# Kernel tuning notes

Hardware: AMD Instinct MI355X
Metric: run time of the kernel (lower is better)

The kernel has to match this reference:

```python
import jax, jax.numpy as jnp
import numpy as np

N_ROLES = 6
EPS = 1e-5

def _ln(x, scale, bias):
    m = jnp.mean(x, axis=-1, keepdims=True)
    v = jnp.var(x, axis=-1, keepdims=True)
    return (x - m) * jax.lax.rsqrt(v + EPS) * scale + bias

def setup_inputs() -> dict:
    key = jax.random.key(0)
    ks = jax.random.split(key, 20)
    T, B, D_OBS, H, A = 32, 1024, 256, 512, 32
    inp = {
        'rnn_states': jax.random.normal(ks[0], (B, H), jnp.float32),
        'obs': jax.random.normal(ks[1], (T, B, D_OBS), jnp.float32),
        'resets': jnp.zeros((T, B), jnp.float32),
        'available_actions': jnp.ones((T, B, A), jnp.float32),
        'role_ids': jax.random.randint(ks[2], (T, B), 0, N_ROLES, jnp.int32),
        # feature norm over obs_dim
        'fn_scale': jnp.ones((D_OBS,), jnp.float32),
        'fn_bias': jnp.zeros((D_OBS,), jnp.float32),
        # base MLP: obs_dim->512->512, each followed by LayerNorm
        'W0': jax.random.normal(ks[3], (D_OBS, H), jnp.float32) * 0.02,
        'b0': jnp.zeros((H,), jnp.float32),
        'ln0_scale': jnp.ones((H,), jnp.float32),
        'ln0_bias': jnp.zeros((H,), jnp.float32),
        'W1': jax.random.normal(ks[4], (H, H), jnp.float32) * 0.02,
        'b1': jnp.zeros((H,), jnp.float32),
        'ln1_scale': jnp.ones((H,), jnp.float32),
        'ln1_bias': jnp.zeros((H,), jnp.float32),
        # per-role routes: obs_dim->128->H (stacked over roles)
        'Wr0': jax.random.normal(ks[5], (N_ROLES, D_OBS, 128), jnp.float32) * 0.02,
        'br0': jnp.zeros((N_ROLES, 128), jnp.float32),
        'Wr1': jax.random.normal(ks[6], (N_ROLES, 128, H), jnp.float32) * 0.02,
        'br1': jnp.zeros((N_ROLES, H), jnp.float32),
        # per-role heads: H->64->32->action_dim (stacked over roles)
        'Wh0': jax.random.normal(ks[7], (N_ROLES, H, 64), jnp.float32) * 0.02,
        'bh0': jnp.zeros((N_ROLES, 64), jnp.float32),
        'Wh1': jax.random.normal(ks[8], (N_ROLES, 64, 32), jnp.float32) * 0.02,
        'bh1': jnp.zeros((N_ROLES, 32), jnp.float32),
        'Wh2': jax.random.normal(ks[9], (N_ROLES, 32, A), jnp.float32) * 0.02,
        'bh2': jnp.zeros((N_ROLES, A), jnp.float32),
    }
    return inp

def _gather_by_role(all_values, role_ids):
    # all_values: (K, T, B, F); role_ids: (T, B) -> (T, B, F)
    idx = role_ids[None, :, :, None].astype(jnp.int32)
    return jnp.take_along_axis(all_values, idx, axis=0)[0]

def reference(rnn_states, obs, resets, available_actions, role_ids,
              fn_scale, fn_bias, W0, b0, ln0_scale, ln0_bias,
              W1, b1, ln1_scale, ln1_bias,
              Wr0, br0, Wr1, br1,
              Wh0, bh0, Wh1, bh1, Wh2, bh2):
    # feature normalization on raw obs
    obs_n = _ln(obs, fn_scale, fn_bias)
    # shared base MLP (relu + LayerNorm after each Dense)
    e = _ln(jax.nn.relu(obs_n @ W0 + b0), ln0_scale, ln0_bias)
    e = _ln(jax.nn.relu(e @ W1 + b1), ln1_scale, ln1_bias)
    # per-role pre-GRU residual routes on (normalized) obs
    r = jax.nn.relu(jnp.einsum('tbi,kih->ktbh', obs_n, Wr0) + br0[:, None, None, :])
    r = jax.nn.relu(jnp.einsum('ktbh,kho->ktbo', r, Wr1) + br1[:, None, None, :])
    e = e + _gather_by_role(r, role_ids)
    # no recurrent policy configured: rnn_states pass through
    # per-role heads -> all logits (K, T, B, A)
    h = jax.nn.relu(jnp.einsum('tbh,khf->ktbf', e, Wh0) + bh0[:, None, None, :])
    h = jax.nn.relu(jnp.einsum('ktbf,kfg->ktbg', h, Wh1) + bh1[:, None, None, :])
    all_logits = jnp.einsum('ktbg,kga->ktba', h, Wh2) + bh2[:, None, None, :]
    logits = _gather_by_role(all_logits, role_ids)
    logits = jnp.where(available_actions > 0.5, logits, jnp.full_like(logits, -1e10))
    return rnn_states, logits
```

## Files before the change

kernel.cpp:

```cpp
#include <hip/hip_runtime.h>
#include <stdint.h>

typedef unsigned short u16;
typedef unsigned int u32;

using bf16x8 = __attribute__((ext_vector_type(8))) short;
using f32x4  = __attribute__((ext_vector_type(4))) float;

#define DEVINL __device__ __forceinline__

DEVINL float b2f(u16 u) { return __builtin_bit_cast(float, (u32)u << 16); }
DEVINL u16 f2b(float f) {
  u32 u = __builtin_bit_cast(u32, f);
  u += 0x7FFFu + ((u >> 16) & 1u);
  return (u16)(u >> 16);
}

DEVINL void gll16(const u16* src, u16* dst) {
  __builtin_amdgcn_global_load_lds(
      (const __attribute__((address_space(1))) void*)(uintptr_t)src,
      (__attribute__((address_space(3))) void*)(uintptr_t)dst, 16, 0, 0);
}

#define MFMA __builtin_amdgcn_mfma_f32_16x16x32_bf16
#define NROLE 6

DEVINL void tp_tile(const float* __restrict__ s, u16* __restrict__ d,
                    int R, int C, int bx, int by, int z)
{
  __shared__ u16 tile[32][33];
  const size_t mstride = (size_t)R * C;
  s += (size_t)z * mstride;
  d += (size_t)z * mstride;
  int r0 = bx * 32, c0 = by * 32;
  int tx = threadIdx.x & 31, ty = threadIdx.x >> 5;
#pragma unroll
  for (int i = 0; i < 32; i += 8)
    tile[ty + i][tx] = f2b(s[(size_t)(r0 + ty + i) * C + (c0 + tx)]);
  __syncthreads();
#pragma unroll
  for (int i = 0; i < 32; i += 8)
    d[(size_t)(c0 + ty + i) * R + (r0 + tx)] = tile[tx][ty + i];
}

__global__ __launch_bounds__(256) void mega0(
    const float* W0, const float* W1, const float* Wr0, const float* Wr1, const float* Wh0,
    u16* W0t, u16* W1t, u16* Wr0t, u16* Wr1t, u16* Wh0t,
    const int* __restrict__ rid, int* __restrict__ blkCnt,
    const float* __restrict__ rnn, float* __restrict__ outRnn)
{
  int b = blockIdx.x;
  const int tid = threadIdx.x;
  if (b < 1152) {
    if (b < 128)      {            tp_tile(W0, W0t, 256, 512, b % 8,  b / 8, 0); }
    else if (b < 384) { b -= 128;  tp_tile(W1, W1t, 512, 512, b % 16, b / 16, 0); }
    else if (b < 576) { b -= 384;  int t = b / 8;  tp_tile(Wr0, Wr0t, 256, 128, b % 8,  t % 4,  t / 4); }
    else if (b < 960) { b -= 576;  int t = b / 4;  tp_tile(Wr1, Wr1t, 128, 512, b % 4,  t % 16, t / 16); }
    else              { b -= 960;  int t = b / 16; tp_tile(Wh0, Wh0t, 512, 64,  b % 16, t % 2,  t / 2); }
  } else if (b < 1280) {
    b -= 1152;
    __shared__ int h[NROLE];
    if (tid < NROLE) h[tid] = 0;
    __syncthreads();
    atomicAdd(&h[rid[b * 256 + tid]], 1);
    __syncthreads();
    if (tid < NROLE) blkCnt[b * NROLE + tid] = h[tid];
  } else {
    b -= 1280;
    const float4* src = (const float4*)rnn;
    float4* dst = (float4*)outRnn;
    int base = (b * 256 + tid) * 4;
#pragma unroll
    for (int i = 0; i < 4; ++i) dst[base + i] = src[base + i];
  }
}

__global__ __launch_bounds__(256, 2) void base2(
    const float* __restrict__ obs, const float* __restrict__ fn_s,
    const float* __restrict__ fn_b, const u16* __restrict__ W0t,
    const float* __restrict__ b0, const float* __restrict__ ln0sc,
    const float* __restrict__ ln0bi, const u16* __restrict__ W1t,
    const float* __restrict__ b1, const float* __restrict__ ln1sc,
    const float* __restrict__ ln1bi, u16* __restrict__ obs_n,
    u16* __restrict__ C,
    const int* __restrict__ rid, const int* __restrict__ blkCnt,
    int* __restrict__ bucket, int* __restrict__ baseArr, int* __restrict__ cntArr)
{
  __shared__ __align__(16) u16 smem[33792];
  const int tid = threadIdx.x;

  if (blockIdx.x >= 512) {
    const int bx = blockIdx.x - 512;
    int* c = (int*)smem;
    int* preArr = c + 768;
    int* scnt   = c + 776;
    int* sbase  = c + 784;
    int* h      = c + 792;
    for (int i = tid; i < 128 * NROLE; i += 256) c[i] = blkCnt[i];
    if (tid < NROLE) h[tid] = 0;
    __syncthreads();
    if (tid < NROLE) {
      int k = tid, run = 0, pre = 0;
      for (int b = 0; b < 128; ++b) { if (b == bx) pre = run; run += c[b * NROLE + k]; }
      scnt[k] = run; preArr[k] = pre;
    }
    __syncthreads();
    if (tid == 0) {
      int r = 0;
      for (int k = 0; k < NROLE; ++k) { sbase[k] = r; r += scnt[k]; }
    }
    __syncthreads();
    if (bx == 0 && tid < NROLE) { baseArr[tid] = sbase[tid]; cntArr[tid] = scnt[tid]; }
    int i = bx * 256 + tid;
    int k = rid[i];
    int pos = atomicAdd(&h[k], 1);
    bucket[sbase[k] + preArr[k] + pos] = i;
    return;
  }

  float* redS  = (float*)&smem[32768];
  float* redSS = redS + 256;
  const int rowBase = blockIdx.x * 64;
  const int lane = tid & 63, wave = tid >> 6;
  const int quad = lane >> 4, lm = lane & 15, l7 = lm & 7;
  const int wn = wave * 128;

  {
    const int r = tid >> 2, q = tid & 3;
    const float* xr = obs + (size_t)(rowBase + r) * 256 + q * 64;
    float x[64];
#pragma unroll
    for (int jj = 0; jj < 16; ++jj)
      *(float4*)&x[jj * 4] = *(const float4*)(xr + jj * 4);
    float s = 0.f, s2 = 0.f;
#pragma unroll
    for (int p = 0; p < 64; ++p) { s += x[p]; s2 += x[p] * x[p]; }
    s  += __shfl_xor(s, 1, 64);  s  += __shfl_xor(s, 2, 64);
    s2 += __shfl_xor(s2, 1, 64); s2 += __shfl_xor(s2, 2, 64);
    float m = s * (1.f / 256.f);
    float var = s2 * (1.f / 256.f) - m * m;
    float inv = rsqrtf(var + 1e-5f);
    const float* fs = fn_s + q * 64;
    const float* fb = fn_b + q * 64;
    u16* og = obs_n + (size_t)(rowBase + r) * 256 + q * 64;
#pragma unroll
    for (int j = 0; j < 8; ++j) {
      float4 fs0 = *(const float4*)(fs + j * 8);
      float4 fs1 = *(const float4*)(fs + j * 8 + 4);
      float4 fb0 = *(const float4*)(fb + j * 8);
      float4 fb1 = *(const float4*)(fb + j * 8 + 4);
      u16 yy[8] __attribute__((aligned(16)));
      yy[0] = f2b((x[j*8+0] - m) * inv * fs0.x + fb0.x);
      yy[1] = f2b((x[j*8+1] - m) * inv * fs0.y + fb0.y);
      yy[2] = f2b((x[j*8+2] - m) * inv * fs0.z + fb0.z);
      yy[3] = f2b((x[j*8+3] - m) * inv * fs0.w + fb0.w);
      yy[4] = f2b((x[j*8+4] - m) * inv * fs1.x + fb1.x);
      yy[5] = f2b((x[j*8+5] - m) * inv * fs1.y + fb1.y);
      yy[6] = f2b((x[j*8+6] - m) * inv * fs1.z + fb1.z);
      yy[7] = f2b((x[j*8+7] - m) * inv * fs1.w + fb1.w);
      int cch = q * 8 + j;
      *(uint4*)&smem[r * 256 + ((cch ^ (r & 7)) * 8)] = *(uint4*)yy;
      *(uint4*)(og + j * 8) = *(uint4*)yy;
    }
  }

  u32 bOff0[8];
#pragma unroll
  for (int j = 0; j < 8; ++j)
    bOff0[j] = (u32)(wn + j * 16 + lm) * 256u + (u32)(quad * 8);
  f32x4 acc[4][8] = {};
  bf16x8 bR[2][8];
#pragma unroll
  for (int p = 0; p < 2; ++p)
#pragma unroll
    for (int j = 0; j < 8; ++j)
      bR[p][j] = *(const bf16x8*)(W0t + bOff0[j] + p * 32);
  __syncthreads();

#pragma unroll
  for (int g = 0; g < 8; ++g) {
    bf16x8 cur[8];
#pragma unroll
    for (int j = 0; j < 8; ++j) cur[j] = bR[g & 1][j];
    if (g + 2 < 8) {
#pragma unroll
      for (int j = 0; j < 8; ++j)
        bR[g & 1][j] = *(const bf16x8*)(W0t + bOff0[j] + (g + 2) * 32);
    }
    const int kc = g * 4;
    bf16x8 af[4];
#pragma unroll
    for (int i2 = 0; i2 < 4; ++i2)
      af[i2] = *(const bf16x8*)&smem[(i2 * 16 + lm) * 256 + (((quad + kc) ^ l7) * 8)];
#pragma unroll
    for (int i2 = 0; i2 < 4; ++i2)
#pragma unroll
      for (int j = 0; j < 8; ++j)
        acc[i2][j] = MFMA(af[i2], cur[j], acc[i2][j], 0, 0, 0);
  }

  {
    float b0v[8];
#pragma unroll
    for (int j = 0; j < 8; ++j) b0v[j] = b0[wn + j * 16 + lm];
#pragma unroll
    for (int i2 = 0; i2 < 4; ++i2) {
#pragma unroll
      for (int r2 = 0; r2 < 4; ++r2) {
        float s = 0.f, ss = 0.f;
#pragma unroll
        for (int j = 0; j < 8; ++j) {
          float v = fmaxf(acc[i2][j][r2] + b0v[j], 0.f);
          acc[i2][j][r2] = v;
          s += v; ss += v * v;
        }
#pragma unroll
        for (int o = 1; o < 16; o <<= 1) { s += __shfl_xor(s, o, 64); ss += __shfl_xor(ss, o, 64); }
        if (lm == 0) {
          int row = i2 * 16 + quad * 4 + r2;
          redS[row * 4 + wave] = s;
          redSS[row * 4 + wave] = ss;
        }
      }
    }
  }
  __syncthreads();

  {
    float s0v[8], s0b[8];
#pragma unroll
    for (int j = 0; j < 8; ++j) {
      s0v[j] = ln0sc[wn + j * 16 + lm];
      s0b[j] = ln0bi[wn + j * 16 + lm];
    }
#pragma unroll
    for (int i2 = 0; i2 < 4; ++i2) {
#pragma unroll
      for (int r2 = 0; r2 < 4; ++r2) {
        int row = i2 * 16 + quad * 4 + r2;
        float ts  = redS[row * 4 + 0] + redS[row * 4 + 1] + redS[row * 4 + 2] + redS[row * 4 + 3];
        float tss = redSS[row * 4 + 0] + redSS[row * 4 + 1] + redSS[row * 4 + 2] + redSS[row * 4 + 3];
        float m = ts * (1.f / 512.f);
        float var = tss * (1.f / 512.f) - m * m;
        float inv = rsqrtf(var + 1e-5f);
#pragma unroll
        for (int j = 0; j < 8; ++j) {
          int col = wn + j * 16 + lm;
          float y = (acc[i2][j][r2] - m) * inv * s0v[j] + s0b[j];
          smem[row * 512 + (((col >> 3) ^ (row & 7)) * 8) + (col & 7)] = f2b(y);
        }
      }
    }
  }
  u32 bOff1[8];
#pragma unroll
  for (int j = 0; j < 8; ++j)
    bOff1[j] = (u32)(wn + j * 16 + lm) * 512u + (u32)(quad * 8);
#pragma unroll
  for (int p = 0; p < 2; ++p)
#pragma unroll
    for (int j = 0; j < 8; ++j)
      bR[p][j] = *(const bf16x8*)(W1t + bOff1[j] + p * 32);
  __syncthreads();

#pragma unroll
  for (int i2 = 0; i2 < 4; ++i2)
#pragma unroll
    for (int j = 0; j < 8; ++j)
      acc[i2][j] = (f32x4){0.f, 0.f, 0.f, 0.f};
#pragma unroll
  for (int g = 0; g < 16; ++g) {
    bf16x8 cur[8];
#pragma unroll
    for (int j = 0; j < 8; ++j) cur[j] = bR[g & 1][j];
    if (g + 2 < 16) {
#pragma unroll
      for (int j = 0; j < 8; ++j)
        bR[g & 1][j] = *(const bf16x8*)(W1t + bOff1[j] + (g + 2) * 32);
    }
    const int kc = g * 4;
    bf16x8 af[4];
#pragma unroll
    for (int i2 = 0; i2 < 4; ++i2)
      af[i2] = *(const bf16x8*)&smem[(i2 * 16 + lm) * 512 + (((quad + kc) ^ l7) * 8)];
#pragma unroll
    for (int i2 = 0; i2 < 4; ++i2)
#pragma unroll
      for (int j = 0; j < 8; ++j)
        acc[i2][j] = MFMA(af[i2], cur[j], acc[i2][j], 0, 0, 0);
  }

  {
    float b1v[8];
#pragma unroll
    for (int j = 0; j < 8; ++j) b1v[j] = b1[wn + j * 16 + lm];
#pragma unroll
    for (int i2 = 0; i2 < 4; ++i2) {
#pragma unroll
      for (int r2 = 0; r2 < 4; ++r2) {
        float s = 0.f, ss = 0.f;
#pragma unroll
        for (int j = 0; j < 8; ++j) {
          float v = fmaxf(acc[i2][j][r2] + b1v[j], 0.f);
          acc[i2][j][r2] = v;
          s += v; ss += v * v;
        }
#pragma unroll
        for (int o = 1; o < 16; o <<= 1) { s += __shfl_xor(s, o, 64); ss += __shfl_xor(ss, o, 64); }
        if (lm == 0) {
          int row = i2 * 16 + quad * 4 + r2;
          redS[row * 4 + wave] = s;
          redSS[row * 4 + wave] = ss;
        }
      }
    }
  }
  __syncthreads();

  {
    float s1v[8], s1b[8];
#pragma unroll
    for (int j = 0; j < 8; ++j) {
      s1v[j] = ln1sc[wn + j * 16 + lm];
      s1b[j] = ln1bi[wn + j * 16 + lm];
    }
#pragma unroll
    for (int i2 = 0; i2 < 4; ++i2) {
#pragma unroll
      for (int r2 = 0; r2 < 4; ++r2) {
        int row = i2 * 16 + quad * 4 + r2;
        float ts  = redS[row * 4 + 0] + redS[row * 4 + 1] + redS[row * 4 + 2] + redS[row * 4 + 3];
        float tss = redSS[row * 4 + 0] + redSS[row * 4 + 1] + redSS[row * 4 + 2] + redSS[row * 4 + 3];
        float m = ts * (1.f / 512.f);
        float var = tss * (1.f / 512.f) - m * m;
        float inv = rsqrtf(var + 1e-5f);
        size_t base = (size_t)(rowBase + row) * 512;
#pragma unroll
        for (int j = 0; j < 8; ++j) {
          int col = wn + j * 16 + lm;
          float y = (acc[i2][j][r2] - m) * inv * s1v[j] + s1b[j];
          C[base + col] = f2b(y);
        }
      }
    }
  }
}

__global__ __launch_bounds__(256, 4) void route_head(
    const u16* __restrict__ obs_n, const u16* __restrict__ e,
    const u16* __restrict__ Wr0t, const float* __restrict__ br0,
    const u16* __restrict__ Wr1t, const float* __restrict__ br1,
    const u16* __restrict__ Wh0t, const float* __restrict__ bh0,
    const float* __restrict__ Wh1, const float* __restrict__ bh1,
    const float* __restrict__ Wh2, const float* __restrict__ bh2,
    const float* __restrict__ avail,
    const int* __restrict__ bucket, const int* __restrict__ baseArr,
    const int* __restrict__ cntArr, float* __restrict__ outLogits)
{
  __shared__ __align__(16) u16 sm[20480];
  const int tid = threadIdx.x;

  int cA0, cA1, cA2, cA3, cA4, cA5, bA0, bA1, bA2, bA3, bA4, bA5;
  {
    int4 ca = *(const int4*)cntArr;  int2 cb = *(const int2*)(cntArr + 4);
    int4 ba = *(const int4*)baseArr; int2 bb = *(const int2*)(baseArr + 4);
    cA0 = ca.x; cA1 = ca.y; cA2 = ca.z; cA3 = ca.w; cA4 = cb.x; cA5 = cb.y;
    bA0 = ba.x; bA1 = ba.y; bA2 = ba.z; bA3 = ba.w; bA4 = bb.x; bA5 = bb.y;
  }
  int role = -1, rem = blockIdx.x, cnt = 0, roleBase = 0;
#define TRY_ROLE(k, ck, bk)                                        \
  if (role < 0) {                                                  \
    int tiles = ((ck) + 31) >> 5;                                  \
    if (rem < tiles) { role = (k); cnt = (ck); roleBase = (bk); }  \
    else rem -= tiles;                                             \
  }
  TRY_ROLE(0, cA0, bA0) TRY_ROLE(1, cA1, bA1) TRY_ROLE(2, cA2, bA2)
  TRY_ROLE(3, cA3, bA3) TRY_ROLE(4, cA4, bA4) TRY_ROLE(5, cA5, bA5)
#undef TRY_ROLE
  if (role < 0) return;
  const int limit = cnt;
  const int rowBase = rem * 32;

  const int lane = tid & 63, wave = tid >> 6;
  const int quad = lane >> 4, lm = lane & 15, l7 = lm & 7;

#pragma unroll
  for (int r = 0; r < 8; ++r) {
    int lrow = r * 4 + wave;
    int i = rowBase + lrow;
    if (i >= limit) i = rowBase;
    int grow = bucket[roleBase + i];
    int chunk = tid & 63;
    int sw = (chunk & 56) | ((chunk ^ lrow) & 7);
    gll16(e + (u32)grow * 512u + (u32)(sw * 8), &sm[r * 2048 + wave * 512]);
  }

  int growA0, growA1;
  {
    int i0 = rowBase + lm;        if (i0 >= limit) i0 = rowBase;
    int i1 = rowBase + 16 + lm;   if (i1 >= limit) i1 = rowBase;
    growA0 = bucket[roleBase + i0];
    growA1 = bucket[roleBase + i1];
  }
  const u16* Ag0 = obs_n + (size_t)growA0 * 256;
  const u16* Ag1 = obs_n + (size_t)growA1 * 256;

  const int wn0 = wave * 32;
  const u16* B0 = Wr0t + (size_t)role * 128 * 256;
  f32x4 acc0[2][2] = {};
  bf16x8 b0R[2][2];
#pragma unroll
  for (int p = 0; p < 2; ++p)
#pragma unroll
    for (int j = 0; j < 2; ++j)
      b0R[p][j] = *(const bf16x8*)(B0 + (u32)(wn0 + j * 16 + lm) * 256u + (u32)(quad * 8 + p * 32));
  bf16x8 aR[4][2];
#pragma unroll
  for (int p = 0; p < 4; ++p) {
    aR[p][0] = *(const bf16x8*)(Ag0 + (u32)(quad * 8 + p * 32));
    aR[p][1] = *(const bf16x8*)(Ag1 + (u32)(quad * 8 + p * 32));
  }
  float bias0[2] = { br0[role * 128 + wn0 + lm], br0[role * 128 + wn0 + 16 + lm] };
#pragma unroll
  for (int it = 0; it < 8; ++it) {
    bf16x8 a0 = aR[it & 3][0], a1 = aR[it & 3][1];
    bf16x8 cur0 = b0R[it & 1][0], cur1 = b0R[it & 1][1];
    if (it + 2 < 8) {
#pragma unroll
      for (int j = 0; j < 2; ++j)
        b0R[it & 1][j] = *(const bf16x8*)(B0 + (u32)(wn0 + j * 16 + lm) * 256u + (u32)(quad * 8 + (it + 2) * 32));
    }
    if (it + 4 < 8) {
      aR[it & 3][0] = *(const bf16x8*)(Ag0 + (u32)(quad * 8 + (it + 4) * 32));
      aR[it & 3][1] = *(const bf16x8*)(Ag1 + (u32)(quad * 8 + (it + 4) * 32));
    }
    acc0[0][0] = MFMA(a0, cur0, acc0[0][0], 0, 0, 0);
    acc0[0][1] = MFMA(a0, cur1, acc0[0][1], 0, 0, 0);
    acc0[1][0] = MFMA(a1, cur0, acc0[1][0], 0, 0, 0);
    acc0[1][1] = MFMA(a1, cur1, acc0[1][1], 0, 0, 0);
  }
  u16* r1 = sm + 16384;
#pragma unroll
  for (int i2 = 0; i2 < 2; ++i2) {
#pragma unroll
    for (int r2 = 0; r2 < 4; ++r2) {
      int row = i2 * 16 + quad * 4 + r2;
#pragma unroll
      for (int j = 0; j < 2; ++j) {
        int col = wn0 + j * 16 + lm;
        float v = fmaxf(acc0[i2][j][r2] + bias0[j], 0.f);
        r1[row * 128 + (((col >> 3) ^ (row & 7)) * 8) + (col & 7)] = f2b(v);
      }
    }
  }
  __syncthreads();

  const int wn1 = wave * 128;
  const u16* B1 = Wr1t + (size_t)role * 512 * 128;
#pragma unroll
  for (int h = 0; h < 2; ++h) {
    const int wnh = wn1 + h * 64;
    float b1v[4];
#pragma unroll
    for (int j = 0; j < 4; ++j) b1v[j] = br1[role * 512 + wnh + j * 16 + lm];
    f32x4 acc1[2][4] = {};
    bf16x8 b1P[4];
#pragma unroll
    for (int j = 0; j < 4; ++j)
      b1P[j] = *(const bf16x8*)(B1 + (u32)(wnh + j * 16 + lm) * 128u + (u32)(quad * 8));
#pragma unroll
    for (int kk = 0; kk < 128; kk += 32) {
      bf16x8 b1N[4];
      if (kk + 32 < 128) {
#pragma unroll
        for (int j = 0; j < 4; ++j)
          b1N[j] = *(const bf16x8*)(B1 + (u32)(wnh + j * 16 + lm) * 128u + (u32)(quad * 8 + kk + 32));
      }
      const int kc = kk >> 3;
      bf16x8 af[2];
#pragma unroll
      for (int i2 = 0; i2 < 2; ++i2)
        af[i2] = *(const bf16x8*)&r1[(i2 * 16 + lm) * 128 + (((quad + kc) ^ l7) * 8)];
#pragma unroll
      for (int i2 = 0; i2 < 2; ++i2)
#pragma unroll
        for (int j = 0; j < 4; ++j)
          acc1[i2][j] = MFMA(af[i2], b1P[j], acc1[i2][j], 0, 0, 0);
      if (kk + 32 < 128) {
#pragma unroll
        for (int j = 0; j < 4; ++j) b1P[j] = b1N[j];
      }
    }
#pragma unroll
    for (int i2 = 0; i2 < 2; ++i2) {
#pragma unroll
      for (int r2 = 0; r2 < 4; ++r2) {
        int row = i2 * 16 + quad * 4 + r2;
#pragma unroll
        for (int j = 0; j < 4; ++j) {
          int col = wnh + j * 16 + lm;
          int addr = row * 512 + (((col >> 3) ^ (row & 7)) * 8) + (col & 7);
          float v = fmaxf(acc1[i2][j][r2] + b1v[j], 0.f) + b2f(sm[addr]);
          sm[addr] = f2b(v);
        }
      }
    }
  }
  __syncthreads();

  const int wn2 = wave * 16;
  const u16* B2 = Wh0t + (size_t)role * 64 * 512;
  float b2v = bh0[role * 64 + wn2 + lm];
  f32x4 acc2[2] = {};
  bf16x8 b2R[4];
#pragma unroll
  for (int p = 0; p < 4; ++p)
    b2R[p] = *(const bf16x8*)(B2 + (u32)(wn2 + lm) * 512u + (u32)(quad * 8 + p * 32));
#pragma unroll
  for (int it = 0; it < 16; ++it) {
    bf16x8 cur = b2R[it & 3];
    if (it + 4 < 16)
      b2R[it & 3] = *(const bf16x8*)(B2 + (u32)(wn2 + lm) * 512u + (u32)(quad * 8 + (it + 4) * 32));
    const int kc = it * 4;
    bf16x8 af[2];
#pragma unroll
    for (int i2 = 0; i2 < 2; ++i2)
      af[i2] = *(const bf16x8*)&sm[(i2 * 16 + lm) * 512 + (((quad + kc) ^ l7) * 8)];
#pragma unroll
    for (int i2 = 0; i2 < 2; ++i2)
      acc2[i2] = MFMA(af[i2], cur, acc2[i2], 0, 0, 0);
  }
  u16* h0s = sm + 16384;
#pragma unroll
  for (int i2 = 0; i2 < 2; ++i2) {
#pragma unroll
    for (int r2 = 0; r2 < 4; ++r2) {
      int row = i2 * 16 + quad * 4 + r2;
      int col = wn2 + lm;
      h0s[row * 68 + col] = f2b(fmaxf(acc2[i2][r2] + b2v, 0.f));
    }
  }
  __syncthreads();

  {
    float* h1s = (float*)&sm[16384];
    const int r = tid >> 3;
    const int n0 = (tid & 7) * 4;
    const bool valid = (rowBase + r) < limit;
    const float* W1k = Wh1 + (size_t)role * 64 * 32;
    const float* W2k = Wh2 + (size_t)role * 32 * 32;
    float4 a1 = *(const float4*)(bh1 + role * 32 + n0);
#pragma unroll 8
    for (int j = 0; j < 64; ++j) {
      float hj = b2f(h0s[r * 68 + j]);
      float4 wv = *(const float4*)(W1k + j * 32 + n0);
      a1.x += hj * wv.x; a1.y += hj * wv.y; a1.z += hj * wv.z; a1.w += hj * wv.w;
    }
    a1.x = fmaxf(a1.x, 0.f); a1.y = fmaxf(a1.y, 0.f);
    a1.z = fmaxf(a1.z, 0.f); a1.w = fmaxf(a1.w, 0.f);
    __syncthreads();
    h1s[r * 36 + n0 + 0] = a1.x;
    h1s[r * 36 + n0 + 1] = a1.y;
    h1s[r * 36 + n0 + 2] = a1.z;
    h1s[r * 36 + n0 + 3] = a1.w;
    __syncthreads();
    float4 a2 = *(const float4*)(bh2 + role * 32 + n0);
#pragma unroll 8
    for (int n = 0; n < 32; ++n) {
      float hn = h1s[r * 36 + n];
      float4 wv = *(const float4*)(W2k + n * 32 + n0);
      a2.x += hn * wv.x; a2.y += hn * wv.y; a2.z += hn * wv.z; a2.w += hn * wv.w;
    }
    if (valid) {
      int g = bucket[roleBase + rowBase + r];
      float4 av = *(const float4*)(avail + (size_t)g * 32 + n0);
      float4 o;
      o.x = (av.x > 0.5f) ? a2.x : -1e10f;
      o.y = (av.y > 0.5f) ? a2.y : -1e10f;
      o.z = (av.z > 0.5f) ? a2.z : -1e10f;
      o.w = (av.w > 0.5f) ? a2.w : -1e10f;
      *(float4*)(outLogits + (size_t)g * 32 + n0) = o;
    }
  }
}

extern "C" void kernel_launch(void* const* d_in, const int* in_sizes, int n_in,
                              void* d_out, int out_size, void* d_ws, size_t ws_size,
                              hipStream_t stream)
{
  const float* rnn  = (const float*)d_in[0];
  const float* obs  = (const float*)d_in[1];
  const float* avail= (const float*)d_in[3];
  const int*   rid  = (const int*)d_in[4];
  const float* fn_s = (const float*)d_in[5];
  const float* fn_b = (const float*)d_in[6];
  const float* W0   = (const float*)d_in[7];
  const float* b0   = (const float*)d_in[8];
  const float* ln0s = (const float*)d_in[9];
  const float* ln0b = (const float*)d_in[10];
  const float* W1   = (const float*)d_in[11];
  const float* b1   = (const float*)d_in[12];
  const float* ln1s = (const float*)d_in[13];
  const float* ln1b = (const float*)d_in[14];
  const float* Wr0  = (const float*)d_in[15];
  const float* br0  = (const float*)d_in[16];
  const float* Wr1  = (const float*)d_in[17];
  const float* br1  = (const float*)d_in[18];
  const float* Wh0  = (const float*)d_in[19];
  const float* bh0  = (const float*)d_in[20];
  const float* Wh1  = (const float*)d_in[21];
  const float* bh1  = (const float*)d_in[22];
  const float* Wh2  = (const float*)d_in[23];
  const float* bh2  = (const float*)d_in[24];

  const int ROWS = 32768;

  char* w = (char*)d_ws;
  auto carve = [&](size_t bytes) { char* p = w; w += (bytes + 255) & ~(size_t)255; return p; };
  u16* obs_n  = (u16*)carve((size_t)ROWS * 256 * 2);
  u16* bufB   = (u16*)carve((size_t)ROWS * 512 * 2);
  u16* W0t    = (u16*)carve((size_t)512 * 256 * 2);
  u16* W1t    = (u16*)carve((size_t)512 * 512 * 2);
  u16* Wr0t   = (u16*)carve((size_t)6 * 128 * 256 * 2);
  u16* Wr1t   = (u16*)carve((size_t)6 * 512 * 128 * 2);
  u16* Wh0t   = (u16*)carve((size_t)6 * 64 * 512 * 2);
  int* bucket = (int*)carve((size_t)ROWS * 4);
  int* blkCnt = (int*)carve((size_t)128 * NROLE * 4);
  int* baseArr= (int*)carve(256);
  int* cntArr = (int*)carve(256);

  float* outLogits = (float*)d_out + (size_t)1024 * 512;

  mega0<<<1408, 256, 0, stream>>>(W0, W1, Wr0, Wr1, Wh0, W0t, W1t, Wr0t, Wr1t, Wh0t,
                                  rid, blkCnt, rnn, (float*)d_out);

  base2<<<640, 256, 0, stream>>>(obs, fn_s, fn_b, W0t, b0, ln0s, ln0b,
                                 W1t, b1, ln1s, ln1b, obs_n, bufB,
                                 rid, blkCnt, bucket, baseArr, cntArr);

  route_head<<<1029, 256, 0, stream>>>(obs_n, bufB, Wr0t, br0, Wr1t, br1, Wh0t, bh0,
                                       Wh1, bh1, Wh2, bh2, avail,
                                       bucket, baseArr, cntArr, outLogits);
}
```

Measured before the change: 263.9 us.

## Halve base MLP row tile to 32 rows for higher occupancy and staged output

The base MLP kernel now processes 32 rows per block instead of 64, using half the shared memory and accumulator registers, with launch bounds raised to 4 blocks per SM and a grid of 1152 blocks. The weight prefetch is reduced from a two-deep register buffer to single-step double buffering. The final LayerNorm output is staged in shared memory and written to global memory with coalesced 16-byte stores. The intent is more resident waves and more blocks to hide latency. The cost is that each block reloads the full W0/W1 weights for fewer rows, doubling weight traffic per output row.

```diff
diff --git a/kernel.cpp b/kernel.cpp
--- a/kernel.cpp
+++ b/kernel.cpp
@@ -75,7 +75,7 @@
   }
 }
 
-__global__ __launch_bounds__(256, 2) void base2(
+__global__ __launch_bounds__(256, 4) void base2v(
     const float* __restrict__ obs, const float* __restrict__ fn_s,
     const float* __restrict__ fn_b, const u16* __restrict__ W0t,
     const float* __restrict__ b0, const float* __restrict__ ln0sc,
@@ -86,11 +86,11 @@
     const int* __restrict__ rid, const int* __restrict__ blkCnt,
     int* __restrict__ bucket, int* __restrict__ baseArr, int* __restrict__ cntArr)
 {
-  __shared__ __align__(16) u16 smem[33792];
+  __shared__ __align__(16) u16 smem[16896];
   const int tid = threadIdx.x;
 
-  if (blockIdx.x >= 512) {
-    const int bx = blockIdx.x - 512;
+  if (blockIdx.x >= 1024) {
+    const int bx = blockIdx.x - 1024;
     int* c = (int*)smem;
     int* preArr = c + 768;
     int* scnt   = c + 776;
@@ -118,33 +118,33 @@
     return;
   }
 
-  float* redS  = (float*)&smem[32768];
-  float* redSS = redS + 256;
-  const int rowBase = blockIdx.x * 64;
+  float* redS  = (float*)&smem[16384];
+  float* redSS = redS + 128;
+  const int rowBase = blockIdx.x * 32;
   const int lane = tid & 63, wave = tid >> 6;
   const int quad = lane >> 4, lm = lane & 15, l7 = lm & 7;
   const int wn = wave * 128;
 
   {
-    const int r = tid >> 2, q = tid & 3;
-    const float* xr = obs + (size_t)(rowBase + r) * 256 + q * 64;
-    float x[64];
-#pragma unroll
-    for (int jj = 0; jj < 16; ++jj)
+    const int r = tid >> 3, q = tid & 7;
+    const float* xr = obs + (size_t)(rowBase + r) * 256 + q * 32;
+    float x[32];
+#pragma unroll
+    for (int jj = 0; jj < 8; ++jj)
       *(float4*)&x[jj * 4] = *(const float4*)(xr + jj * 4);
     float s = 0.f, s2 = 0.f;
 #pragma unroll
-    for (int p = 0; p < 64; ++p) { s += x[p]; s2 += x[p] * x[p]; }
-    s  += __shfl_xor(s, 1, 64);  s  += __shfl_xor(s, 2, 64);
-    s2 += __shfl_xor(s2, 1, 64); s2 += __shfl_xor(s2, 2, 64);
+    for (int p = 0; p < 32; ++p) { s += x[p]; s2 += x[p] * x[p]; }
+    s  += __shfl_xor(s, 1, 64);  s  += __shfl_xor(s, 2, 64);  s  += __shfl_xor(s, 4, 64);
+    s2 += __shfl_xor(s2, 1, 64); s2 += __shfl_xor(s2, 2, 64); s2 += __shfl_xor(s2, 4, 64);
     float m = s * (1.f / 256.f);
     float var = s2 * (1.f / 256.f) - m * m;
     float inv = rsqrtf(var + 1e-5f);
-    const float* fs = fn_s + q * 64;
-    const float* fb = fn_b + q * 64;
-    u16* og = obs_n + (size_t)(rowBase + r) * 256 + q * 64;
-#pragma unroll
-    for (int j = 0; j < 8; ++j) {
+    const float* fs = fn_s + q * 32;
+    const float* fb = fn_b + q * 32;
+    u16* og = obs_n + (size_t)(rowBase + r) * 256 + q * 32;
+#pragma unroll
+    for (int j = 0; j < 4; ++j) {
       float4 fs0 = *(const float4*)(fs + j * 8);
       float4 fs1 = *(const float4*)(fs + j * 8 + 4);
       float4 fb0 = *(const float4*)(fb + j * 8);
@@ -158,45 +158,45 @@
       yy[5] = f2b((x[j*8+5] - m) * inv * fs1.y + fb1.y);
       yy[6] = f2b((x[j*8+6] - m) * inv * fs1.z + fb1.z);
       yy[7] = f2b((x[j*8+7] - m) * inv * fs1.w + fb1.w);
-      int cch = q * 8 + j;
+      int cch = q * 4 + j;
       *(uint4*)&smem[r * 256 + ((cch ^ (r & 7)) * 8)] = *(uint4*)yy;
       *(uint4*)(og + j * 8) = *(uint4*)yy;
     }
   }
+  __syncthreads();
 
   u32 bOff0[8];
 #pragma unroll
   for (int j = 0; j < 8; ++j)
     bOff0[j] = (u32)(wn + j * 16 + lm) * 256u + (u32)(quad * 8);
-  f32x4 acc[4][8] = {};
-  bf16x8 bR[2][8];
-#pragma unroll
-  for (int p = 0; p < 2; ++p)
-#pragma unroll
-    for (int j = 0; j < 8; ++j)
-      bR[p][j] = *(const bf16x8*)(W0t + bOff0[j] + p * 32);
-  __syncthreads();
-
-#pragma unroll
-  for (int g = 0; g < 8; ++g) {
-    bf16x8 cur[8];
-#pragma unroll
-    for (int j = 0; j < 8; ++j) cur[j] = bR[g & 1][j];
-    if (g + 2 < 8) {
-#pragma unroll
-      for (int j = 0; j < 8; ++j)
-        bR[g & 1][j] = *(const bf16x8*)(W0t + bOff0[j] + (g + 2) * 32);
-    }
-    const int kc = g * 4;
-    bf16x8 af[4];
-#pragma unroll
-    for (int i2 = 0; i2 < 4; ++i2)
-      af[i2] = *(const bf16x8*)&smem[(i2 * 16 + lm) * 256 + (((quad + kc) ^ l7) * 8)];
-#pragma unroll
-    for (int i2 = 0; i2 < 4; ++i2)
-#pragma unroll
-      for (int j = 0; j < 8; ++j)
-        acc[i2][j] = MFMA(af[i2], cur[j], acc[i2][j], 0, 0, 0);
+  f32x4 acc[2][8] = {};
+  {
+    bf16x8 bP[8];
+#pragma unroll
+    for (int j = 0; j < 8; ++j) bP[j] = *(const bf16x8*)(W0t + bOff0[j]);
+#pragma unroll
+    for (int g = 0; g < 8; ++g) {
+      bf16x8 bN[8];
+      if (g + 1 < 8) {
+#pragma unroll
+        for (int j = 0; j < 8; ++j)
+          bN[j] = *(const bf16x8*)(W0t + bOff0[j] + (g + 1) * 32);
+      }
+      const int kc = g * 4;
+      bf16x8 af[2];
+#pragma unroll
+      for (int i2 = 0; i2 < 2; ++i2)
+        af[i2] = *(const bf16x8*)&smem[(i2 * 16 + lm) * 256 + (((quad + kc) ^ l7) * 8)];
+#pragma unroll
+      for (int i2 = 0; i2 < 2; ++i2)
+#pragma unroll
+        for (int j = 0; j < 8; ++j)
+          acc[i2][j] = MFMA(af[i2], bP[j], acc[i2][j], 0, 0, 0);
+      if (g + 1 < 8) {
+#pragma unroll
+        for (int j = 0; j < 8; ++j) bP[j] = bN[j];
+      }
+    }
   }
 
   {
@@ -204,7 +204,7 @@
 #pragma unroll
     for (int j = 0; j < 8; ++j) b0v[j] = b0[wn + j * 16 + lm];
 #pragma unroll
-    for (int i2 = 0; i2 < 4; ++i2) {
+    for (int i2 = 0; i2 < 2; ++i2) {
 #pragma unroll
       for (int r2 = 0; r2 < 4; ++r2) {
         float s = 0.f, ss = 0.f;
@@ -234,7 +234,7 @@
       s0b[j] = ln0bi[wn + j * 16 + lm];
     }
 #pragma unroll
-    for (int i2 = 0; i2 < 4; ++i2) {
+    for (int i2 = 0; i2 < 2; ++i2) {
 #pragma unroll
       for (int r2 = 0; r2 < 4; ++r2) {
         int row = i2 * 16 + quad * 4 + r2;
@@ -252,42 +252,44 @@
       }
     }
   }
+  __syncthreads();
+
   u32 bOff1[8];
 #pragma unroll
   for (int j = 0; j < 8; ++j)
     bOff1[j] = (u32)(wn + j * 16 + lm) * 512u + (u32)(quad * 8);
 #pragma unroll
-  for (int p = 0; p < 2; ++p)
-#pragma unroll
-    for (int j = 0; j < 8; ++j)
-      bR[p][j] = *(const bf16x8*)(W1t + bOff1[j] + p * 32);
-  __syncthreads();
-
-#pragma unroll
-  for (int i2 = 0; i2 < 4; ++i2)
+  for (int i2 = 0; i2 < 2; ++i2)
 #pragma unroll
     for (int j = 0; j < 8; ++j)
       acc[i2][j] = (f32x4){0.f, 0.f, 0.f, 0.f};
-#pragma unroll
-  for (int g = 0; g < 16; ++g) {
-    bf16x8 cur[8];
-#pragma unroll
-    for (int j = 0; j < 8; ++j) cur[j] = bR[g & 1][j];
-    if (g + 2 < 16) {
-#pragma unroll
-      for (int j = 0; j < 8; ++j)
-        bR[g & 1][j] = *(const bf16x8*)(W1t + bOff1[j] + (g + 2) * 32);
-    }
-    const int kc = g * 4;
-    bf16x8 af[4];
-#pragma unroll
-    for (int i2 = 0; i2 < 4; ++i2)
-      af[i2] = *(const bf16x8*)&smem[(i2 * 16 + lm) * 512 + (((quad + kc) ^ l7) * 8)];
-#pragma unroll
-    for (int i2 = 0; i2 < 4; ++i2)
-#pragma unroll
-      for (int j = 0; j < 8; ++j)
-        acc[i2][j] = MFMA(af[i2], cur[j], acc[i2][j], 0, 0, 0);
+  {
+    bf16x8 bP[8];
+#pragma unroll
+    for (int j = 0; j < 8; ++j) bP[j] = *(const bf16x8*)(W1t + bOff1[j]);
+#pragma unroll
+    for (int g = 0; g < 16; ++g) {
+      bf16x8 bN[8];
+      if (g + 1 < 16) {
+#pragma unroll
+        for (int j = 0; j < 8; ++j)
+          bN[j] = *(const bf16x8*)(W1t + bOff1[j] + (g + 1) * 32);
+      }
+      const int kc = g * 4;
+      bf16x8 af[2];
+#pragma unroll
+      for (int i2 = 0; i2 < 2; ++i2)
+        af[i2] = *(const bf16x8*)&smem[(i2 * 16 + lm) * 512 + (((quad + kc) ^ l7) * 8)];
+#pragma unroll
+      for (int i2 = 0; i2 < 2; ++i2)
+#pragma unroll
+        for (int j = 0; j < 8; ++j)
+          acc[i2][j] = MFMA(af[i2], bP[j], acc[i2][j], 0, 0, 0);
+      if (g + 1 < 16) {
+#pragma unroll
+        for (int j = 0; j < 8; ++j) bP[j] = bN[j];
+      }
+    }
   }
 
   {
@@ -295,7 +297,7 @@
 #pragma unroll
     for (int j = 0; j < 8; ++j) b1v[j] = b1[wn + j * 16 + lm];
 #pragma unroll
-    for (int i2 = 0; i2 < 4; ++i2) {
+    for (int i2 = 0; i2 < 2; ++i2) {
 #pragma unroll
       for (int r2 = 0; r2 < 4; ++r2) {
         float s = 0.f, ss = 0.f;
@@ -325,7 +327,7 @@
       s1b[j] = ln1bi[wn + j * 16 + lm];
     }
 #pragma unroll
-    for (int i2 = 0; i2 < 4; ++i2) {
+    for (int i2 = 0; i2 < 2; ++i2) {
 #pragma unroll
       for (int r2 = 0; r2 < 4; ++r2) {
         int row = i2 * 16 + quad * 4 + r2;
@@ -334,14 +336,23 @@
         float m = ts * (1.f / 512.f);
         float var = tss * (1.f / 512.f) - m * m;
         float inv = rsqrtf(var + 1e-5f);
-        size_t base = (size_t)(rowBase + row) * 512;
 #pragma unroll
         for (int j = 0; j < 8; ++j) {
           int col = wn + j * 16 + lm;
           float y = (acc[i2][j][r2] - m) * inv * s1v[j] + s1b[j];
-          C[base + col] = f2b(y);
+          smem[row * 512 + col] = f2b(y);
         }
       }
+    }
+  }
+  __syncthreads();
+
+  {
+    u16* dst = C + (size_t)rowBase * 512;
+#pragma unroll
+    for (int it = 0; it < 8; ++it) {
+      int idx = (it * 256 + tid) * 8;
+      *(uint4*)(dst + idx) = *(const uint4*)&smem[idx];
     }
   }
 }
@@ -634,9 +645,9 @@
   mega0<<<1408, 256, 0, stream>>>(W0, W1, Wr0, Wr1, Wh0, W0t, W1t, Wr0t, Wr1t, Wh0t,
                                   rid, blkCnt, rnn, (float*)d_out);
 
-  base2<<<640, 256, 0, stream>>>(obs, fn_s, fn_b, W0t, b0, ln0s, ln0b,
-                                 W1t, b1, ln1s, ln1b, obs_n, bufB,
-                                 rid, blkCnt, bucket, baseArr, cntArr);
+  base2v<<<1152, 256, 0, stream>>>(obs, fn_s, fn_b, W0t, b0, ln0s, ln0b,
+                                   W1t, b1, ln1s, ln1b, obs_n, bufB,
+                                   rid, blkCnt, bucket, baseArr, cntArr);
 
   route_head<<<1029, 256, 0, stream>>>(obs_n, bufB, Wr0t, br0, Wr1t, br1, Wh0t, bh0,
                                        Wh1, bh1, Wh2, bh2, avail,
```

Result: slower. 302.6 us (+14.7%).
